# Optimization experiments

Hardware: AMD Instinct MI355X
Metric: run time of the kernel (lower is better)

The kernel has to match this reference:

```python
import jax, jax.numpy as jnp
import numpy as np

EMBED_DIM = 768
NUM_HEADS = 12
HEAD_DIM = EMBED_DIM // NUM_HEADS
SCALE = HEAD_DIM ** -0.5
B, N = 8, 1024


def setup_inputs() -> dict:
    key = jax.random.key(0)
    ks = jax.random.split(key, 5)
    return {
        "x": jax.random.normal(ks[0], (B, N, EMBED_DIM), dtype=jnp.float32),
        "qkv_w": jax.random.normal(ks[1], (3 * EMBED_DIM, EMBED_DIM), dtype=jnp.float32) * 0.02,
        "qkv_b": jax.random.normal(ks[2], (3 * EMBED_DIM,), dtype=jnp.float32) * 0.02,
        "proj_w": jax.random.normal(ks[3], (EMBED_DIM, EMBED_DIM), dtype=jnp.float32) * 0.02,
        "proj_b": jax.random.normal(ks[4], (EMBED_DIM,), dtype=jnp.float32) * 0.02,
    }


def reference(x, qkv_w, qkv_b, proj_w, proj_b):
    b, n, c = x.shape
    h, hd = NUM_HEADS, HEAD_DIM
    # QKV projection: [b,n,3c]
    qkv = jnp.einsum("bnc,dc->bnd", x, qkv_w) + qkv_b
    qkv = qkv.reshape(b, n, 3, h, hd).transpose(2, 0, 3, 1, 4)  # [3,b,h,n,hd]
    q, k, v = qkv[0], qkv[1], qkv[2]
    # scaled dot-product attention (eager path; dropout is identity in eval)
    attn = jnp.einsum("bhqd,bhkd->bhqk", q, k) * SCALE
    attn = jax.nn.softmax(attn, axis=-1)
    out = jnp.einsum("bhqk,bhkd->bhqd", attn, v)  # [b,h,n,hd]
    out = out.transpose(0, 2, 1, 3).reshape(b, n, c)
    # output projection
    return jnp.einsum("bnc,dc->bnd", out, proj_w) + proj_b
```

## Files before the change

kernel.cpp:

```cpp
#include <hip/hip_runtime.h>
#include <hip/hip_bf16.h>

typedef __attribute__((ext_vector_type(4))) float f32x4;
typedef __attribute__((ext_vector_type(8))) short short8;
typedef unsigned short u16;

#define MFMA(a, b, c) __builtin_amdgcn_mfma_f32_16x16x32_bf16((a), (b), (c), 0, 0, 0)

#define WAITVM_BAR(N) do {                                          \
    asm volatile("s_waitcnt vmcnt(" #N ")" ::: "memory");           \
    __builtin_amdgcn_s_barrier();                                   \
    __builtin_amdgcn_sched_barrier(0);                              \
} while (0)
#define BAR2() do {                                                 \
    __builtin_amdgcn_sched_barrier(0);                              \
    __builtin_amdgcn_s_barrier();                                   \
    __builtin_amdgcn_sched_barrier(0);                              \
} while (0)

static constexpr int EMBED = 768;
static constexpr int NH = 12;
static constexpr int HD = 64;
static constexpr int BATCH = 8;
static constexpr int SEQ = 1024;

__device__ __forceinline__ u16 f2bu(float f) {
    __hip_bfloat16 h = __float2bfloat16(f);
    u16 u; __builtin_memcpy(&u, &h, 2); return u;
}
__device__ __forceinline__ float exp2a(float x) {
    float r; asm("v_exp_f32 %0, %1" : "=v"(r) : "v"(x)); return r;
}
__device__ __forceinline__ unsigned cvt_pk_bf16(float lo, float hi) {
    unsigned r; asm("v_cvt_pk_bf16_f32 %0, %1, %2" : "=v"(r) : "v"(lo), "v"(hi)); return r;
}
__device__ __forceinline__ float max3f(float a, float b, float c) {
    return fmaxf(fmaxf(a, b), c);
}
__device__ __forceinline__ void swap32(unsigned& a, unsigned& b) {
    asm volatile("v_permlane32_swap_b32 %0, %1" : "+v"(a), "+v"(b));
}
__device__ __forceinline__ void swap16(unsigned& a, unsigned& b) {
    asm volatile("v_permlane16_swap_b32 %0, %1" : "+v"(a), "+v"(b));
}
__device__ __forceinline__ short8 mk8(unsigned w0, unsigned w1, unsigned w2, unsigned w3) {
    union { unsigned u[4]; short8 s; } c;
    c.u[0] = w0; c.u[1] = w1; c.u[2] = w2; c.u[3] = w3;
    return c.s;
}

__global__ void cvt_all_k(const float* __restrict__ x, const float* __restrict__ w1,
                          const float* __restrict__ w2,
                          u16* __restrict__ xb, u16* __restrict__ wb, u16* __restrict__ pw) {
    const int n1 = BATCH * SEQ * EMBED;
    const int n2 = 3 * EMBED * EMBED;
    const int n3 = EMBED * EMBED;
    int i = (blockIdx.x * blockDim.x + threadIdx.x) * 4;
    const float* src; u16* dst;
    if (i < n1)            { src = x  + i;             dst = xb + i; }
    else if (i < n1 + n2)  { src = w1 + (i - n1);      dst = wb + (i - n1); }
    else if (i < n1+n2+n3) { src = w2 + (i - n1 - n2); dst = pw + (i - n1 - n2); }
    else return;
    float4 v = *reinterpret_cast<const float4*>(src);
    ushort4 o;
    o.x = f2bu(v.x); o.y = f2bu(v.y); o.z = f2bu(v.z); o.w = f2bu(v.w);
    *reinterpret_cast<ushort4*>(dst) = o;
}

template <int EPI>
__global__ __launch_bounds__(256)
void gemm_bt_k(const u16* __restrict__ A, const u16* __restrict__ Bw,
               const float* __restrict__ bias,
               u16* __restrict__ q_out, u16* __restrict__ k_out,
               u16* __restrict__ vt_out, float* __restrict__ f_out)
{
    __shared__ __attribute__((aligned(16))) char smem[65536];
    const int tid  = threadIdx.x;
    const int wave = tid >> 6, lane = tid & 63;
    const int hi   = lane >> 4, l15 = lane & 15;
    const int wr   = wave >> 1, wc = wave & 1;
    const int bm   = blockIdx.x, bn = blockIdx.y;

    f32x4 acc[4][4] = {};

    const size_t arow0 = (size_t)bm * 128;
    const size_t brow0 = (size_t)bn * 128;

    auto stage = [&](int buf, int kt) {
        char* Ab = smem + buf * 32768;
        char* Bb = Ab + 16384;
#pragma unroll
        for (int c = 0; c < 4; ++c) {
            int ck   = c * 4 + wave;
            int p    = ck * 1024 + lane * 16;
            int row  = p >> 7;
            int pcol = (p & 127) ^ ((row & 7) << 4);
            const u16* srcA = A  + (arow0 + row) * EMBED + kt + (pcol >> 1);
            const u16* srcB = Bw + (brow0 + row) * EMBED + kt + (pcol >> 1);
            __builtin_amdgcn_global_load_lds((const __attribute__((address_space(1))) void*)srcA,
                                             (__attribute__((address_space(3))) void*)(Ab + ck * 1024), 16, 0, 0);
            __builtin_amdgcn_global_load_lds((const __attribute__((address_space(1))) void*)srcB,
                                             (__attribute__((address_space(3))) void*)(Bb + ck * 1024), 16, 0, 0);
        }
    };

    auto comp = [&](const char* Ab, const char* Bb) {
#pragma unroll
        for (int kk = 0; kk < 2; ++kk) {
            short8 af[4], bf[4];
#pragma unroll
            for (int mi = 0; mi < 4; ++mi) {
                int R  = wr * 64 + mi * 16 + l15;
                int Cb = kk * 64 + hi * 16;
                af[mi] = *reinterpret_cast<const short8*>(Ab + R * 128 + (Cb ^ ((R & 7) << 4)));
            }
#pragma unroll
            for (int ni = 0; ni < 4; ++ni) {
                int R  = wc * 64 + ni * 16 + l15;
                int Cb = kk * 64 + hi * 16;
                bf[ni] = *reinterpret_cast<const short8*>(Bb + R * 128 + (Cb ^ ((R & 7) << 4)));
            }
#pragma unroll
            for (int mi = 0; mi < 4; ++mi)
#pragma unroll
                for (int ni = 0; ni < 4; ++ni)
                    acc[mi][ni] = MFMA(af[mi], bf[ni], acc[mi][ni]);
        }
    };

    const char* A0 = smem;
    const char* B0 = smem + 16384;
    const char* A1 = smem + 32768;
    const char* B1 = smem + 49152;

    stage(0, 0);
#pragma unroll
    for (int tt = 0; tt < 5; ++tt) {
        stage(1, (2 * tt + 1) * 64);
        WAITVM_BAR(8);
        comp(A0, B0);
        BAR2();
        stage(0, (2 * tt + 2) * 64);
        WAITVM_BAR(8);
        comp(A1, B1);
        BAR2();
    }
    stage(1, 11 * 64);
    WAITVM_BAR(8);
    comp(A0, B0);
    BAR2();
    WAITVM_BAR(0);
    comp(A1, B1);

#pragma unroll
    for (int mi = 0; mi < 4; ++mi) {
        int crow0 = bm * 128 + wr * 64 + mi * 16 + hi * 4;
#pragma unroll
        for (int ni = 0; ni < 4; ++ni) {
            int ccol = bn * 128 + wc * 64 + ni * 16 + l15;
            float bv = bias[ccol];
            if constexpr (EPI == 0) {
                int which = ccol / 768;
                int rem   = ccol - which * 768;
                int hh = rem >> 6, hd = rem & 63;
                int bb = crow0 >> 10, nn0 = crow0 & 1023;
                size_t bh = (size_t)(bb * NH + hh);
                if (which == 2) {
                    uint2 pk;
                    pk.x = cvt_pk_bf16(acc[mi][ni][0] + bv, acc[mi][ni][1] + bv);
                    pk.y = cvt_pk_bf16(acc[mi][ni][2] + bv, acc[mi][ni][3] + bv);
                    *reinterpret_cast<uint2*>(&vt_out[(bh * HD + hd) * SEQ + nn0]) = pk;
                } else if (which == 0) {
#pragma unroll
                    for (int r = 0; r < 4; ++r)
                        q_out[(bh * SEQ + nn0 + r) * HD + hd] =
                            f2bu((acc[mi][ni][r] + bv) * 0.18033688f);
                } else {
#pragma unroll
                    for (int r = 0; r < 4; ++r)
                        k_out[(bh * SEQ + nn0 + r) * HD + hd] = f2bu(acc[mi][ni][r] + bv);
                }
            } else {
#pragma unroll
                for (int r = 0; r < 4; ++r)
                    f_out[(size_t)(crow0 + r) * EMBED + ccol] = acc[mi][ni][r] + bv;
            }
        }
    }
}

__global__ __launch_bounds__(512, 6)
void attn_k(const u16* __restrict__ Q, const u16* __restrict__ K,
            const u16* __restrict__ Vt, u16* __restrict__ AO)
{
    __shared__ __attribute__((aligned(16))) u16 kls[3][4096];
    __shared__ __attribute__((aligned(16))) u16 vls[3][4096];

    const int tid = threadIdx.x;
    const int w   = tid >> 6, lane = tid & 63;
    const int hi  = lane >> 4, l15 = lane & 15;
    const int f   = blockIdx.x;
    const int xcd = f & 7, i = f >> 3;
    const int bh  = xcd * 12 + (i % 12);
    const int q0w = (i / 12) * 128 + w * 16;

    const u16* Qh = Q  + (size_t)bh * SEQ * HD;
    const u16* Kh = K  + (size_t)bh * SEQ * HD;
    const u16* Vh = Vt + (size_t)bh * HD * SEQ;

    const int sp    = w * 1024 + lane * 16;
    const int srow  = sp >> 7;
    const int scolb = (sp & 127) ^ ((srow & 7) << 4);
    const u16* kbase = Kh + (size_t)srow * HD + (scolb >> 1);
    const u16* vbase = Vh + (size_t)srow * SEQ + (scolb >> 1);

    auto stage = [&](u16* kdst, u16* vdst, int t) {
        __builtin_amdgcn_global_load_lds(
            (const __attribute__((address_space(1))) void*)(kbase + (size_t)t * 64 * HD),
            (__attribute__((address_space(3))) void*)(kdst + w * 512), 16, 0, 0);
        __builtin_amdgcn_global_load_lds(
            (const __attribute__((address_space(1))) void*)(vbase + (size_t)t * 64),
            (__attribute__((address_space(3))) void*)(vdst + w * 512), 16, 0, 0);
    };

    short8 qf[2];
#pragma unroll
    for (int dh = 0; dh < 2; ++dh)
        qf[dh] = *reinterpret_cast<const short8*>(
            Qh + (size_t)(q0w + l15) * HD + dh * 32 + hi * 8);
    __builtin_amdgcn_sched_barrier(0);

    stage(kls[0], vls[0], 0);
    stage(kls[1], vls[1], 1);

    f32x4 accO[4] = {};
    float m = -1e30f, lp = 0.f;

    auto tile = [&](const u16* Kb, const u16* Vb) {
        f32x4 st[4] = {};
        __builtin_amdgcn_s_setprio(1);
#pragma unroll
        for (int kb = 0; kb < 4; ++kb) {
            int R  = kb * 16 + l15;
            int sw = (R & 7) << 4;
            short8 kf0 = *reinterpret_cast<const short8*>(Kb + R * 64 + (((hi * 16) ^ sw) >> 1));
            short8 kf1 = *reinterpret_cast<const short8*>(Kb + R * 64 + (((64 + hi * 16) ^ sw) >> 1));
            st[kb] = MFMA(kf0, qf[0], st[kb]);
            st[kb] = MFMA(kf1, qf[1], st[kb]);
        }
        __builtin_amdgcn_s_setprio(0);

        float t0 = max3f(st[0][0], st[0][1], st[0][2]);
        float t1 = max3f(st[0][3], st[1][0], st[1][1]);
        float t2 = max3f(st[1][2], st[1][3], st[2][0]);
        float t3 = max3f(st[2][1], st[2][2], st[2][3]);
        float t4 = max3f(st[3][0], st[3][1], st[3][2]);
        float tm = fmaxf(max3f(t0, t1, t2), max3f(t3, t4, st[3][3]));
        tm = fmaxf(tm, __shfl_xor(tm, 16, 64));
        tm = fmaxf(tm, __shfl_xor(tm, 32, 64));
        if (!__all(tm <= m + 8.f)) {
            float mn = fmaxf(m, tm);
            float sc = exp2a(m - mn);
            m = mn;
            lp *= sc;
#pragma unroll
            for (int db = 0; db < 4; ++db)
#pragma unroll
                for (int r = 0; r < 4; ++r) accO[db][r] *= sc;
        }

        unsigned X[4][2];
#pragma unroll
        for (int kb = 0; kb < 4; ++kb) {
            float e0 = exp2a(st[kb][0] - m);
            float e1 = exp2a(st[kb][1] - m);
            float e2 = exp2a(st[kb][2] - m);
            float e3 = exp2a(st[kb][3] - m);
            lp += (e0 + e1) + (e2 + e3);
            X[kb][0] = cvt_pk_bf16(e0, e1);
            X[kb][1] = cvt_pk_bf16(e2, e3);
        }

        unsigned a0 = X[0][0], b0 = X[1][0];
        swap32(a0, b0); swap16(a0, b0);
        unsigned a1 = X[0][1], b1 = X[1][1];
        swap32(a1, b1); swap16(a1, b1);
        unsigned a2 = X[2][0], b2 = X[3][0];
        swap32(a2, b2); swap16(a2, b2);
        unsigned a3 = X[2][1], b3 = X[3][1];
        swap32(a3, b3); swap16(a3, b3);
        short8 pa0 = mk8(a0, a1, b0, b1);
        short8 pa1 = mk8(a2, a3, b2, b3);

        __builtin_amdgcn_s_setprio(1);
#pragma unroll
        for (int db = 0; db < 4; ++db) {
            int R  = db * 16 + l15;
            int sw = (R & 7) << 4;
            short8 vf0 = *reinterpret_cast<const short8*>(Vb + R * 64 + (((hi * 16) ^ sw) >> 1));
            short8 vf1 = *reinterpret_cast<const short8*>(Vb + R * 64 + (((64 + hi * 16) ^ sw) >> 1));
            accO[db] = MFMA(vf0, pa0, accO[db]);
            accO[db] = MFMA(vf1, pa1, accO[db]);
        }
        __builtin_amdgcn_s_setprio(0);
    };

    auto one = [&](const u16* Kc, const u16* Vc, u16* Ks, u16* Vs, int tn, bool ds) {
        asm volatile("s_waitcnt vmcnt(2)" ::: "memory");
        __builtin_amdgcn_s_barrier();
        __builtin_amdgcn_sched_barrier(0);
        if (ds) stage(Ks, Vs, tn);
        tile(Kc, Vc);
        __builtin_amdgcn_sched_barrier(0);
    };

    for (int g = 0; g < 5; ++g) {
        one(kls[0], vls[0], kls[2], vls[2], 3 * g + 2, true);
        one(kls[1], vls[1], kls[0], vls[0], 3 * g + 3, 3 * g + 3 <= 15);
        one(kls[2], vls[2], kls[1], vls[1], 3 * g + 4, 3 * g + 4 <= 15);
    }
    asm volatile("s_waitcnt vmcnt(0)" ::: "memory");
    __builtin_amdgcn_s_barrier();
    __builtin_amdgcn_sched_barrier(0);
    tile(kls[0], vls[0]);

    lp += __shfl_xor(lp, 16, 64);
    lp += __shfl_xor(lp, 32, 64);
    float linv = 1.f / lp;
    const int bb = bh / NH, hh = bh - bb * NH;
    size_t rowb = ((size_t)bb * SEQ + q0w + l15) * EMBED + hh * HD;
#pragma unroll
    for (int db = 0; db < 4; ++db) {
        float o0 = accO[db][0] * linv, o1 = accO[db][1] * linv;
        float o2 = accO[db][2] * linv, o3 = accO[db][3] * linv;
        uint2 pkd;
        pkd.x = cvt_pk_bf16(o0, o1);
        pkd.y = cvt_pk_bf16(o2, o3);
        *reinterpret_cast<uint2*>(&AO[rowb + db * 16 + hi * 4]) = pkd;
    }
}

extern "C" void kernel_launch(void* const* d_in, const int* in_sizes, int n_in,
                              void* d_out, int out_size, void* d_ws, size_t ws_size,
                              hipStream_t stream)
{
    const float* x      = (const float*)d_in[0];
    const float* qkv_w  = (const float*)d_in[1];
    const float* qkv_b  = (const float*)d_in[2];
    const float* proj_w = (const float*)d_in[3];
    const float* proj_b = (const float*)d_in[4];
    float* out = (float*)d_out;

    char* ws = (char*)d_ws;
    u16* xb  = (u16*)(ws);
    u16* wb  = (u16*)(ws + 12582912);
    u16* pw  = (u16*)(ws + 16121856);
    u16* qb  = (u16*)(ws + 17301504);
    u16* kb  = (u16*)(ws + 29884416);
    u16* vt  = (u16*)(ws + 42467328);
    u16* ao  = (u16*)(ws + 55050240);

    cvt_all_k<<<8448, 256, 0, stream>>>(x, qkv_w, proj_w, xb, wb, pw);

    gemm_bt_k<0><<<dim3(64, 18), 256, 0, stream>>>(xb, wb, qkv_b, qb, kb, vt, nullptr);
    attn_k<<<768, 512, 0, stream>>>(qb, kb, vt, ao);
    gemm_bt_k<1><<<dim3(64, 6), 256, 0, stream>>>(ao, pw, proj_b, nullptr, nullptr, nullptr, out);
}
```

Before: 103.8 us.

## Process two query tiles per wave in attention to reuse K/V fragments

The attention kernel moves from 8 waves with 16 query rows each to 4 waves with 32 query rows each, so every K and V fragment read from LDS feeds two MFMA chains. Each wave now stages twice as many K/V chunks per tile. The online-softmax rescale now runs after the PV MFMAs, and the running max is set from the first tile instead of -inf. The aim is to cut LDS reads per FLOP and barrier overhead, at the cost of more registers per thread and fewer waves in flight to hide latency.

Result: no change. 103.3 us (-0.5%).

```diff
diff --git a/kernel.cpp b/kernel.cpp
--- a/kernel.cpp
+++ b/kernel.cpp
@@ -189,12 +189,11 @@
     }
 }
 
-__global__ __launch_bounds__(512, 6)
+__global__ __launch_bounds__(256, 3)
 void attn_k(const u16* __restrict__ Q, const u16* __restrict__ K,
             const u16* __restrict__ Vt, u16* __restrict__ AO)
 {
-    __shared__ __attribute__((aligned(16))) u16 kls[3][4096];
-    __shared__ __attribute__((aligned(16))) u16 vls[3][4096];
+    __shared__ __attribute__((aligned(16))) u16 kv[3][8192];
 
     const int tid = threadIdx.x;
     const int w   = tid >> 6, lane = tid & 63;
@@ -202,42 +201,48 @@
     const int f   = blockIdx.x;
     const int xcd = f & 7, i = f >> 3;
     const int bh  = xcd * 12 + (i % 12);
-    const int q0w = (i / 12) * 128 + w * 16;
+    const int q0w = (i / 12) * 128 + w * 32;
 
     const u16* Qh = Q  + (size_t)bh * SEQ * HD;
     const u16* Kh = K  + (size_t)bh * SEQ * HD;
     const u16* Vh = Vt + (size_t)bh * HD * SEQ;
 
-    const int sp    = w * 1024 + lane * 16;
-    const int srow  = sp >> 7;
-    const int scolb = (sp & 127) ^ ((srow & 7) << 4);
-    const u16* kbase = Kh + (size_t)srow * HD + (scolb >> 1);
-    const u16* vbase = Vh + (size_t)srow * SEQ + (scolb >> 1);
-
-    auto stage = [&](u16* kdst, u16* vdst, int t) {
-        __builtin_amdgcn_global_load_lds(
-            (const __attribute__((address_space(1))) void*)(kbase + (size_t)t * 64 * HD),
-            (__attribute__((address_space(3))) void*)(kdst + w * 512), 16, 0, 0);
-        __builtin_amdgcn_global_load_lds(
-            (const __attribute__((address_space(1))) void*)(vbase + (size_t)t * 64),
-            (__attribute__((address_space(3))) void*)(vdst + w * 512), 16, 0, 0);
+    short8 qf[2][2];
+#pragma unroll
+    for (int qh = 0; qh < 2; ++qh)
+#pragma unroll
+        for (int dh = 0; dh < 2; ++dh)
+            qf[qh][dh] = *reinterpret_cast<const short8*>(
+                Qh + (size_t)(q0w + qh * 16 + l15) * HD + dh * 32 + hi * 8);
+    __builtin_amdgcn_sched_barrier(0);
+
+    const u16* sptr[4]; int doff[4]; int sadv[4];
+#pragma unroll
+    for (int c = 0; c < 4; ++c) {
+        int ch = c * 4 + w;
+        int mc = ch & 7;
+        int p  = mc * 1024 + lane * 16;
+        int row = p >> 7;
+        int colb = (p & 127) ^ ((row & 7) << 4);
+        if (ch < 8) { sptr[c] = Kh + (size_t)row * HD + (colb >> 1); sadv[c] = 64 * HD; doff[c] = mc * 512; }
+        else        { sptr[c] = Vh + (size_t)row * SEQ + (colb >> 1); sadv[c] = 64;     doff[c] = 4096 + mc * 512; }
+    }
+    auto stage = [&](int buf, int t) {
+#pragma unroll
+        for (int c = 0; c < 4; ++c)
+            __builtin_amdgcn_global_load_lds(
+                (const __attribute__((address_space(1))) void*)(sptr[c] + (size_t)t * sadv[c]),
+                (__attribute__((address_space(3))) void*)(&kv[buf][doff[c]]), 16, 0, 0);
     };
 
-    short8 qf[2];
-#pragma unroll
-    for (int dh = 0; dh < 2; ++dh)
-        qf[dh] = *reinterpret_cast<const short8*>(
-            Qh + (size_t)(q0w + l15) * HD + dh * 32 + hi * 8);
-    __builtin_amdgcn_sched_barrier(0);
-
-    stage(kls[0], vls[0], 0);
-    stage(kls[1], vls[1], 1);
-
-    f32x4 accO[4] = {};
-    float m = -1e30f, lp = 0.f;
-
-    auto tile = [&](const u16* Kb, const u16* Vb) {
-        f32x4 st[4] = {};
+    stage(0, 0);
+    stage(1, 1);
+
+    f32x4 accO0[4] = {}, accO1[4] = {};
+    float m0 = 0.f, m1 = 0.f, lp0 = 0.f, lp1 = 0.f;
+
+    auto tile = [&](const u16* Kb, const u16* Vb, bool first) {
+        f32x4 st0[4] = {}, st1[4] = {};
         __builtin_amdgcn_s_setprio(1);
 #pragma unroll
         for (int kb = 0; kb < 4; ++kb) {
@@ -245,52 +250,70 @@
             int sw = (R & 7) << 4;
             short8 kf0 = *reinterpret_cast<const short8*>(Kb + R * 64 + (((hi * 16) ^ sw) >> 1));
             short8 kf1 = *reinterpret_cast<const short8*>(Kb + R * 64 + (((64 + hi * 16) ^ sw) >> 1));
-            st[kb] = MFMA(kf0, qf[0], st[kb]);
-            st[kb] = MFMA(kf1, qf[1], st[kb]);
+            st0[kb] = MFMA(kf0, qf[0][0], st0[kb]);
+            st0[kb] = MFMA(kf1, qf[0][1], st0[kb]);
+            st1[kb] = MFMA(kf0, qf[1][0], st1[kb]);
+            st1[kb] = MFMA(kf1, qf[1][1], st1[kb]);
         }
         __builtin_amdgcn_s_setprio(0);
 
-        float t0 = max3f(st[0][0], st[0][1], st[0][2]);
-        float t1 = max3f(st[0][3], st[1][0], st[1][1]);
-        float t2 = max3f(st[1][2], st[1][3], st[2][0]);
-        float t3 = max3f(st[2][1], st[2][2], st[2][3]);
-        float t4 = max3f(st[3][0], st[3][1], st[3][2]);
-        float tm = fmaxf(max3f(t0, t1, t2), max3f(t3, t4, st[3][3]));
-        tm = fmaxf(tm, __shfl_xor(tm, 16, 64));
-        tm = fmaxf(tm, __shfl_xor(tm, 32, 64));
-        if (!__all(tm <= m + 8.f)) {
-            float mn = fmaxf(m, tm);
-            float sc = exp2a(m - mn);
-            m = mn;
-            lp *= sc;
-#pragma unroll
-            for (int db = 0; db < 4; ++db)
-#pragma unroll
-                for (int r = 0; r < 4; ++r) accO[db][r] *= sc;
-        }
-
-        unsigned X[4][2];
+        float a0 = max3f(st0[0][0], st0[0][1], st0[0][2]);
+        float a1 = max3f(st0[0][3], st0[1][0], st0[1][1]);
+        float a2 = max3f(st0[1][2], st0[1][3], st0[2][0]);
+        float a3 = max3f(st0[2][1], st0[2][2], st0[2][3]);
+        float a4 = max3f(st0[3][0], st0[3][1], st0[3][2]);
+        float tm0 = fmaxf(max3f(a0, a1, a2), max3f(a3, a4, st0[3][3]));
+        float b0 = max3f(st1[0][0], st1[0][1], st1[0][2]);
+        float b1 = max3f(st1[0][3], st1[1][0], st1[1][1]);
+        float b2 = max3f(st1[1][2], st1[1][3], st1[2][0]);
+        float b3 = max3f(st1[2][1], st1[2][2], st1[2][3]);
+        float b4 = max3f(st1[3][0], st1[3][1], st1[3][2]);
+        float tm1 = fmaxf(max3f(b0, b1, b2), max3f(b3, b4, st1[3][3]));
+        tm0 = fmaxf(tm0, __shfl_xor(tm0, 16, 64));
+        tm0 = fmaxf(tm0, __shfl_xor(tm0, 32, 64));
+        tm1 = fmaxf(tm1, __shfl_xor(tm1, 16, 64));
+        tm1 = fmaxf(tm1, __shfl_xor(tm1, 32, 64));
+        if (first) { m0 = tm0; m1 = tm1; }
+
+        unsigned X0[4][2], X1[4][2];
 #pragma unroll
         for (int kb = 0; kb < 4; ++kb) {
-            float e0 = exp2a(st[kb][0] - m);
-            float e1 = exp2a(st[kb][1] - m);
-            float e2 = exp2a(st[kb][2] - m);
-            float e3 = exp2a(st[kb][3] - m);
-            lp += (e0 + e1) + (e2 + e3);
-            X[kb][0] = cvt_pk_bf16(e0, e1);
-            X[kb][1] = cvt_pk_bf16(e2, e3);
-        }
-
-        unsigned a0 = X[0][0], b0 = X[1][0];
-        swap32(a0, b0); swap16(a0, b0);
-        unsigned a1 = X[0][1], b1 = X[1][1];
-        swap32(a1, b1); swap16(a1, b1);
-        unsigned a2 = X[2][0], b2 = X[3][0];
-        swap32(a2, b2); swap16(a2, b2);
-        unsigned a3 = X[2][1], b3 = X[3][1];
-        swap32(a3, b3); swap16(a3, b3);
-        short8 pa0 = mk8(a0, a1, b0, b1);
-        short8 pa1 = mk8(a2, a3, b2, b3);
+            float e0 = exp2a(st0[kb][0] - m0);
+            float e1 = exp2a(st0[kb][1] - m0);
+            float e2 = exp2a(st0[kb][2] - m0);
+            float e3 = exp2a(st0[kb][3] - m0);
+            lp0 += (e0 + e1) + (e2 + e3);
+            X0[kb][0] = cvt_pk_bf16(e0, e1);
+            X0[kb][1] = cvt_pk_bf16(e2, e3);
+            float g0 = exp2a(st1[kb][0] - m1);
+            float g1 = exp2a(st1[kb][1] - m1);
+            float g2 = exp2a(st1[kb][2] - m1);
+            float g3 = exp2a(st1[kb][3] - m1);
+            lp1 += (g0 + g1) + (g2 + g3);
+            X1[kb][0] = cvt_pk_bf16(g0, g1);
+            X1[kb][1] = cvt_pk_bf16(g2, g3);
+        }
+
+        unsigned c0 = X0[0][0], d0 = X0[1][0];
+        swap32(c0, d0); swap16(c0, d0);
+        unsigned c1 = X0[0][1], d1 = X0[1][1];
+        swap32(c1, d1); swap16(c1, d1);
+        unsigned c2 = X0[2][0], d2 = X0[3][0];
+        swap32(c2, d2); swap16(c2, d2);
+        unsigned c3 = X0[2][1], d3 = X0[3][1];
+        swap32(c3, d3); swap16(c3, d3);
+        short8 pa00 = mk8(c0, c1, d0, d1);
+        short8 pa01 = mk8(c2, c3, d2, d3);
+        unsigned e0 = X1[0][0], f0 = X1[1][0];
+        swap32(e0, f0); swap16(e0, f0);
+        unsigned e1 = X1[0][1], f1 = X1[1][1];
+        swap32(e1, f1); swap16(e1, f1);
+        unsigned e2 = X1[2][0], f2 = X1[3][0];
+        swap32(e2, f2); swap16(e2, f2);
+        unsigned e3 = X1[2][1], f3 = X1[3][1];
+        swap32(e3, f3); swap16(e3, f3);
+        short8 pa10 = mk8(e0, e1, f0, f1);
+        short8 pa11 = mk8(e2, e3, f2, f3);
 
         __builtin_amdgcn_s_setprio(1);
 #pragma unroll
@@ -299,44 +322,64 @@
             int sw = (R & 7) << 4;
             short8 vf0 = *reinterpret_cast<const short8*>(Vb + R * 64 + (((hi * 16) ^ sw) >> 1));
             short8 vf1 = *reinterpret_cast<const short8*>(Vb + R * 64 + (((64 + hi * 16) ^ sw) >> 1));
-            accO[db] = MFMA(vf0, pa0, accO[db]);
-            accO[db] = MFMA(vf1, pa1, accO[db]);
+            accO0[db] = MFMA(vf0, pa00, accO0[db]);
+            accO0[db] = MFMA(vf1, pa01, accO0[db]);
+            accO1[db] = MFMA(vf0, pa10, accO1[db]);
+            accO1[db] = MFMA(vf1, pa11, accO1[db]);
         }
         __builtin_amdgcn_s_setprio(0);
+
+        if (!first && !__all((tm0 <= m0 + 8.f) && (tm1 <= m1 + 8.f))) {
+            float mn0 = fmaxf(m0, tm0), mn1 = fmaxf(m1, tm1);
+            float s0 = exp2a(m0 - mn0), s1 = exp2a(m1 - mn1);
+            m0 = mn0; m1 = mn1;
+            lp0 *= s0; lp1 *= s1;
+#pragma unroll
+            for (int db = 0; db < 4; ++db)
+#pragma unroll
+                for (int r = 0; r < 4; ++r) { accO0[db][r] *= s0; accO1[db][r] *= s1; }
+        }
     };
 
-    auto one = [&](const u16* Kc, const u16* Vc, u16* Ks, u16* Vs, int tn, bool ds) {
-        asm volatile("s_waitcnt vmcnt(2)" ::: "memory");
+    auto one = [&](int bc, int bs, int tn, bool ds, bool first) {
+        asm volatile("s_waitcnt vmcnt(4)" ::: "memory");
         __builtin_amdgcn_s_barrier();
         __builtin_amdgcn_sched_barrier(0);
-        if (ds) stage(Ks, Vs, tn);
-        tile(Kc, Vc);
+        if (ds) stage(bs, tn);
+        tile(&kv[bc][0], &kv[bc][4096], first);
         __builtin_amdgcn_sched_barrier(0);
     };
 
-    for (int g = 0; g < 5; ++g) {
-        one(kls[0], vls[0], kls[2], vls[2], 3 * g + 2, true);
-        one(kls[1], vls[1], kls[0], vls[0], 3 * g + 3, 3 * g + 3 <= 15);
-        one(kls[2], vls[2], kls[1], vls[1], 3 * g + 4, 3 * g + 4 <= 15);
+    one(0, 2, 2, true, true);
+    one(1, 0, 3, true, false);
+    one(2, 1, 4, true, false);
+    for (int g = 1; g < 5; ++g) {
+        one(0, 2, 3 * g + 2, true, false);
+        one(1, 0, 3 * g + 3, 3 * g + 3 <= 15, false);
+        one(2, 1, 3 * g + 4, 3 * g + 4 <= 15, false);
     }
     asm volatile("s_waitcnt vmcnt(0)" ::: "memory");
     __builtin_amdgcn_s_barrier();
     __builtin_amdgcn_sched_barrier(0);
-    tile(kls[0], vls[0]);
-
-    lp += __shfl_xor(lp, 16, 64);
-    lp += __shfl_xor(lp, 32, 64);
-    float linv = 1.f / lp;
+    tile(&kv[0][0], &kv[0][4096], false);
+
+    lp0 += __shfl_xor(lp0, 16, 64);
+    lp0 += __shfl_xor(lp0, 32, 64);
+    lp1 += __shfl_xor(lp1, 16, 64);
+    lp1 += __shfl_xor(lp1, 32, 64);
+    float linv0 = 1.f / lp0, linv1 = 1.f / lp1;
     const int bb = bh / NH, hh = bh - bb * NH;
-    size_t rowb = ((size_t)bb * SEQ + q0w + l15) * EMBED + hh * HD;
+    size_t rowb0 = ((size_t)bb * SEQ + q0w + l15) * EMBED + hh * HD;
+    size_t rowb1 = rowb0 + (size_t)16 * EMBED;
 #pragma unroll
     for (int db = 0; db < 4; ++db) {
-        float o0 = accO[db][0] * linv, o1 = accO[db][1] * linv;
-        float o2 = accO[db][2] * linv, o3 = accO[db][3] * linv;
-        uint2 pkd;
-        pkd.x = cvt_pk_bf16(o0, o1);
-        pkd.y = cvt_pk_bf16(o2, o3);
-        *reinterpret_cast<uint2*>(&AO[rowb + db * 16 + hi * 4]) = pkd;
+        uint2 pk0, pk1;
+        pk0.x = cvt_pk_bf16(accO0[db][0] * linv0, accO0[db][1] * linv0);
+        pk0.y = cvt_pk_bf16(accO0[db][2] * linv0, accO0[db][3] * linv0);
+        pk1.x = cvt_pk_bf16(accO1[db][0] * linv1, accO1[db][1] * linv1);
+        pk1.y = cvt_pk_bf16(accO1[db][2] * linv1, accO1[db][3] * linv1);
+        *reinterpret_cast<uint2*>(&AO[rowb0 + db * 16 + hi * 4]) = pk0;
+        *reinterpret_cast<uint2*>(&AO[rowb1 + db * 16 + hi * 4]) = pk1;
     }
 }
 
@@ -363,6 +406,6 @@
     cvt_all_k<<<8448, 256, 0, stream>>>(x, qkv_w, proj_w, xb, wb, pw);
 
     gemm_bt_k<0><<<dim3(64, 18), 256, 0, stream>>>(xb, wb, qkv_b, qb, kb, vt, nullptr);
-    attn_k<<<768, 512, 0, stream>>>(qb, kb, vt, ao);
+    attn_k<<<768, 256, 0, stream>>>(qb, kb, vt, ao);
     gemm_bt_k<1><<<dim3(64, 6), 256, 0, stream>>>(ao, pw, proj_b, nullptr, nullptr, nullptr, out);
 }
```
